# Performance work log

Hardware: AMD Instinct MI355X
Metric: run time of the kernel (lower is better)

## Reference

```python
import jax, jax.numpy as jnp
import numpy as np

N_NODES = 50000
N_EDGES = 800000
IN_CH = 64
HID = 128  # hidden_dim_conv == hidden_dim_readout


def setup_inputs() -> dict:
    key = jax.random.key(0)
    ks = jax.random.split(key, 16)
    x = jax.random.normal(ks[0], (N_NODES, 1, IN_CH), dtype=jnp.float32)
    edge_index = jax.random.randint(ks[1], (2, N_EDGES), 0, N_NODES, dtype=jnp.int64)
    edge_weight = jax.random.uniform(ks[2], (N_EDGES,), dtype=jnp.float32)

    def lin(k, out_d, in_d):
        s = 1.0 / np.sqrt(in_d)
        return jax.random.uniform(k, (out_d, in_d), minval=-s, maxval=s, dtype=jnp.float32)

    params = {
        "W_rel0": lin(ks[3], HID, IN_CH), "b_rel0": jnp.zeros((HID,), jnp.float32),
        "W_root0": lin(ks[4], HID, IN_CH),
        "W_ro0": lin(ks[5], HID, HID), "b_ro0": jnp.zeros((HID,), jnp.float32),
        "W_rel1": lin(ks[6], HID, HID), "b_rel1": jnp.zeros((HID,), jnp.float32),
        "W_root1": lin(ks[7], HID, HID),
        "W_ro1": lin(ks[8], HID, HID), "b_ro1": jnp.zeros((HID,), jnp.float32),
        "W_prd": lin(ks[9], 1, HID), "b_prd": jnp.zeros((1,), jnp.float32),
    }
    return {"dynamic_node_features": x, "edge_index": edge_index, "edge_weight": edge_weight, **params}


def reference(dynamic_node_features, edge_index, edge_weight,
              W_rel0, b_rel0, W_root0, W_ro0, b_ro0,
              W_rel1, b_rel1, W_root1, W_ro1, b_ro1,
              W_prd, b_prd):
    # Dropout layers are identity at inference.
    src, dst = edge_index[0], edge_index[1]
    n = dynamic_node_features.shape[0]
    # in-degree counts for 'mean' aggregation (nodes with no in-edges -> 0 output)
    counts = jax.ops.segment_sum(jnp.ones((edge_weight.shape[0],), edge_weight.dtype), dst, num_segments=n)
    denom = jnp.maximum(counts, 1.0)[:, None]  # [N,1]

    def graph_conv(h, W_rel, b_rel, W_root):
        # PyG GraphConv: lin_rel(mean_j edge_weight_ij * h_j) + lin_root(h_i)
        msg = edge_weight[:, None] * h[src]                       # [E,C]
        agg = jax.ops.segment_sum(msg, dst, num_segments=n) / denom  # [N,C]
        return agg @ W_rel.T + b_rel + h @ W_root.T

    h = dynamic_node_features[:, 0, :]                            # [N,IN_CH]
    h = jax.nn.relu(graph_conv(h, W_rel0, b_rel0, W_root0))
    h = jax.nn.relu(h @ W_ro0.T + b_ro0)                          # readout layer 0
    h = jax.nn.relu(graph_conv(h, W_rel1, b_rel1, W_root1))
    h = jax.nn.relu(h @ W_ro1.T + b_ro1)                          # readout layer 1
    out = h @ W_prd.T + b_prd                                     # [N,1]
    return out[:, None, :]                                        # [N,1,1]
```

## Files before the change

kernel.cpp:

```cpp
#include <hip/hip_runtime.h>
#include <hip/hip_fp16.h>

#define N_NODES 50000
#define N_EDGES 800000
#define IN_CH 64
#define HID 128
#define MAXDEG 64
#define CHUNK 6250

typedef __attribute__((ext_vector_type(8))) short bf16x8;
typedef __attribute__((ext_vector_type(8))) _Float16 f16x8;
typedef __attribute__((ext_vector_type(4))) float f32x4;

__device__ __forceinline__ unsigned pack_split(float v) {
    unsigned u = __float_as_uint(v);
    unsigned hi = (u + 0x7fffu + ((u >> 16) & 1u)) & 0xffff0000u;
    float r = v - __uint_as_float(hi);
    unsigned ur = __float_as_uint(r);
    unsigned lo = ((ur + 0x7fffu + ((ur >> 16) & 1u)) >> 16) & 0xffffu;
    return hi | lo;
}


__global__ __launch_bounds__(256) void count_fill_pack(
    const int* __restrict__ src, const int* __restrict__ dst,
    const float* __restrict__ w, int* __restrict__ cnt, int2* __restrict__ csr, int e,
    const float* __restrict__ x, __half* __restrict__ xh, int nx,
    const float* __restrict__ w_rel0, const float* __restrict__ w_root0,
    const float* __restrict__ w_ro0, const float* __restrict__ w_rel1,
    const float* __restrict__ w_root1, const float* __restrict__ w_ro1,
    unsigned short* __restrict__ hi, unsigned short* __restrict__ lo,
    unsigned short* __restrict__ rhi, unsigned short* __restrict__ rlo) {
    const int cls = (int)blockIdx.x & 7;
    const int slice = (int)blockIdx.x >> 3;
    const int nsl = (int)gridDim.x >> 3;
    const int tid = (int)(blockIdx.x * blockDim.x + threadIdx.x);

    for (int i = slice * 256 + (int)threadIdx.x; i < e; i += nsl * 256) {
        int d = dst[i];
        if (d / CHUNK != cls) continue;
        int r = atomicAdd(&cnt[d], 1);
        if (r < MAXDEG) {
            unsigned long long v =
                ((unsigned long long)(unsigned)__float_as_uint(w[i]) << 32) | (unsigned)src[i];
            __builtin_nontemporal_store(v, (unsigned long long*)&csr[(size_t)d * MAXDEG + r]);
        }
    }

    int i4 = tid * 4;
    if (i4 + 3 < nx) {
        float4 v = *(const float4*)&x[i4];
        __half2 a = __floats2half2_rn(v.x, v.y);
        __half2 b = __floats2half2_rn(v.z, v.w);
        uint2 o;
        o.x = *(unsigned*)&a;
        o.y = *(unsigned*)&b;
        *(uint2*)&xh[i4] = o;
    }

    if (tid < 81920) {
        const float* srcw;
        int li;
        if (tid < 8192) { srcw = w_rel0; li = tid; }
        else if (tid < 16384) { srcw = w_root0; li = tid - 8192; }
        else if (tid < 32768) { srcw = w_ro0; li = tid - 16384; }
        else if (tid < 49152) { srcw = w_rel1; li = tid - 32768; }
        else if (tid < 65536) { srcw = w_root1; li = tid - 49152; }
        else { srcw = w_ro1; li = tid - 65536; }
        unsigned p = pack_split(srcw[li]);
        hi[tid] = (unsigned short)(p >> 16);
        lo[tid] = (unsigned short)(p & 0xffffu);
    } else if (tid < 90112) {
        int li = tid - 81920;
        float v = w_root0[li];
        __half h = __float2half(v);
        __half l = __float2half(v - __half2float(h));
        rhi[li] = __half_as_ushort(h);
        rlo[li] = __half_as_ushort(l);
    } else if (tid < 106496) {
        int li = tid - 90112;
        float v = w_root1[li];
        __half h = __float2half(v);
        __half l = __float2half(v - __half2float(h));
        rhi[8192 + li] = __half_as_ushort(h);
        rlo[8192 + li] = __half_as_ushort(l);
    }
}


__global__ void aggregate64(const __half2* __restrict__ xh2, const int* __restrict__ cnt,
                            const int2* __restrict__ csr,
                            unsigned* __restrict__ agg, int n) {
    int tid = blockIdx.x * blockDim.x + threadIdx.x;
    int lane = tid & 63;
    int sl = lane & 31;
    int node = ((tid >> 6) << 1) + (lane >> 5);
    if (node >= n) return;
    int deg = cnt[node];
    int end = deg < MAXDEG ? deg : MAXDEG;
    float inv = 1.0f / fmaxf((float)deg, 1.0f);
    const int2* cp = csr + (size_t)node * MAXDEG;
    float ax = 0.0f, ay = 0.0f;
    int e = 0;
    for (; e + 16 <= end; e += 16) {
        int2 p[16];
        __half2 v[16];
#pragma unroll
        for (int q = 0; q < 16; ++q) p[q] = cp[e + q];
#pragma unroll
        for (int q = 0; q < 16; ++q) v[q] = xh2[(size_t)p[q].x * 32 + sl];
#pragma unroll
        for (int q = 0; q < 16; ++q) {
            float wv = __int_as_float(p[q].y);
            float2 f = __half22float2(v[q]);
            ax += wv * f.x;
            ay += wv * f.y;
        }
    }
    for (; e + 4 <= end; e += 4) {
        int2 p[4];
        __half2 v[4];
#pragma unroll
        for (int q = 0; q < 4; ++q) p[q] = cp[e + q];
#pragma unroll
        for (int q = 0; q < 4; ++q) v[q] = xh2[(size_t)p[q].x * 32 + sl];
#pragma unroll
        for (int q = 0; q < 4; ++q) {
            float wv = __int_as_float(p[q].y);
            float2 f = __half22float2(v[q]);
            ax += wv * f.x;
            ay += wv * f.y;
        }
    }
    for (; e < end; ++e) {
        int2 p = cp[e];
        float wv = __int_as_float(p.y);
        float2 f = __half22float2(xh2[(size_t)p.x * 32 + sl]);
        ax += wv * f.x;
        ay += wv * f.y;
    }
    uint2 o;
    o.x = pack_split(ax * inv);
    o.y = pack_split(ay * inv);
    ((uint2*)agg)[(size_t)node * 32 + sl] = o;
}

__global__ void aggregate128(const uint2* __restrict__ h2h, const int* __restrict__ cnt,
                             const int2* __restrict__ csr,
                             unsigned* __restrict__ agg, int n) {
    int tid = blockIdx.x * blockDim.x + threadIdx.x;
    int lane = tid & 63;
    int sl = lane & 31;
    int node = ((tid >> 6) << 1) + (lane >> 5);
    if (node >= n) return;
    int deg = cnt[node];
    int end = deg < MAXDEG ? deg : MAXDEG;
    float inv = 1.0f / fmaxf((float)deg, 1.0f);
    const int2* cp = csr + (size_t)node * MAXDEG;
    float ax = 0.0f, ay = 0.0f, az = 0.0f, aw = 0.0f;
    int e = 0;
    for (; e + 8 <= end; e += 8) {
        int2 p[8];
        uint2 v[8];
#pragma unroll
        for (int q = 0; q < 8; ++q) p[q] = cp[e + q];
#pragma unroll
        for (int q = 0; q < 8; ++q) v[q] = h2h[(size_t)p[q].x * 32 + sl];
#pragma unroll
        for (int q = 0; q < 8; ++q) {
            float wv = __int_as_float(p[q].y);
            float2 f0 = __half22float2(*(const __half2*)&v[q].x);
            float2 f1 = __half22float2(*(const __half2*)&v[q].y);
            ax += wv * f0.x;
            ay += wv * f0.y;
            az += wv * f1.x;
            aw += wv * f1.y;
        }
    }
    for (; e < end; ++e) {
        int2 p = cp[e];
        float wv = __int_as_float(p.y);
        uint2 v = h2h[(size_t)p.x * 32 + sl];
        float2 f0 = __half22float2(*(const __half2*)&v.x);
        float2 f1 = __half22float2(*(const __half2*)&v.y);
        ax += wv * f0.x;
        ay += wv * f0.y;
        az += wv * f1.x;
        aw += wv * f1.y;
    }
    uint4 o;
    o.x = pack_split(ax * inv);
    o.y = pack_split(ay * inv);
    o.z = pack_split(az * inv);
    o.w = pack_split(aw * inv);
    *(uint4*)&agg[(size_t)node * 128 + sl * 4] = o;
}


template <int K1, int EMIT2>
__global__ __launch_bounds__(256) void gemm_fused(
    const unsigned* __restrict__ A0,
    const unsigned short* __restrict__ W0Hi, const unsigned short* __restrict__ W0Lo,
    const __half* __restrict__ A1h,
    const unsigned short* __restrict__ W1fHi, const unsigned short* __restrict__ W1fLo,
    const float* __restrict__ bias1,
    const unsigned short* __restrict__ W2Hi, const unsigned short* __restrict__ W2Lo,
    const float* __restrict__ bias2,
    __half* __restrict__ Yh,
    const float* __restrict__ pred_w, const float* __restrict__ pred_b,
    float* __restrict__ pred_out, int n) {
    constexpr int KS1 = K1 / 32;
    constexpr int KS2 = 128 / 32;
    const int lane = (int)threadIdx.x & 63;
    const int wv = (int)threadIdx.x >> 6;
    const int col = lane & 15;
    const int quad = lane >> 4;

    __shared__ unsigned h1s[16][132];
    __shared__ float pp[4][16];

    bf16x8 wh1[2][KS1], wl1[2][KS1];
    f16x8 wf1h[2][KS1], wf1l[2][KS1];
    bf16x8 wh2[2][KS2], wl2[2][KS2];
#pragma unroll
    for (int tt = 0; tt < 2; ++tt) {
        const int j = (2 * wv + tt) * 16 + col;
#pragma unroll
        for (int ks = 0; ks < KS1; ++ks) {
            const size_t wo = (size_t)j * K1 + ks * 32 + quad * 8;
            wh1[tt][ks] = *(const bf16x8*)&W0Hi[wo];
            wl1[tt][ks] = *(const bf16x8*)&W0Lo[wo];
            wf1h[tt][ks] = *(const f16x8*)&W1fHi[wo];
            wf1l[tt][ks] = *(const f16x8*)&W1fLo[wo];
        }
#pragma unroll
        for (int ks = 0; ks < KS2; ++ks) {
            const size_t wo = (size_t)j * 128 + ks * 32 + quad * 8;
            wh2[tt][ks] = *(const bf16x8*)&W2Hi[wo];
            wl2[tt][ks] = *(const bf16x8*)&W2Lo[wo];
        }
    }

    float bb1[2], bb2[2], wpv[2];
#pragma unroll
    for (int tt = 0; tt < 2; ++tt) {
        bb1[tt] = bias1[(2 * wv + tt) * 16 + col];
        bb2[tt] = bias2[(2 * wv + tt) * 16 + col];
        if constexpr (EMIT2 == 2) wpv[tt] = pred_w[(2 * wv + tt) * 16 + col];
    }

    const int ngroups = (n + 15) >> 4;
    for (int g = (int)blockIdx.x; g < ngroups; g += (int)gridDim.x) {
        const int m0 = g * 16;
        int arow = m0 + col;
        if (arow >= n) arow = n - 1;

        f32x4 acc[2];
#pragma unroll
        for (int tt = 0; tt < 2; ++tt) acc[tt] = (f32x4){0.f, 0.f, 0.f, 0.f};
#pragma unroll
        for (int ks = 0; ks < KS1; ++ks) {
            const unsigned* ap = &A0[(size_t)arow * K1 + ks * 32 + quad * 8];
            uint4 q0 = *(const uint4*)ap;
            uint4 q1 = *(const uint4*)(ap + 4);
            bf16x8 ahi, alo;
            ahi[0] = (short)(q0.x >> 16); alo[0] = (short)(q0.x & 0xffffu);
            ahi[1] = (short)(q0.y >> 16); alo[1] = (short)(q0.y & 0xffffu);
            ahi[2] = (short)(q0.z >> 16); alo[2] = (short)(q0.z & 0xffffu);
            ahi[3] = (short)(q0.w >> 16); alo[3] = (short)(q0.w & 0xffffu);
            ahi[4] = (short)(q1.x >> 16); alo[4] = (short)(q1.x & 0xffffu);
            ahi[5] = (short)(q1.y >> 16); alo[5] = (short)(q1.y & 0xffffu);
            ahi[6] = (short)(q1.z >> 16); alo[6] = (short)(q1.z & 0xffffu);
            ahi[7] = (short)(q1.w >> 16); alo[7] = (short)(q1.w & 0xffffu);
#pragma unroll
            for (int tt = 0; tt < 2; ++tt) {
                acc[tt] = __builtin_amdgcn_mfma_f32_16x16x32_bf16(ahi, wh1[tt][ks], acc[tt], 0, 0, 0);
                acc[tt] = __builtin_amdgcn_mfma_f32_16x16x32_bf16(ahi, wl1[tt][ks], acc[tt], 0, 0, 0);
                acc[tt] = __builtin_amdgcn_mfma_f32_16x16x32_bf16(alo, wh1[tt][ks], acc[tt], 0, 0, 0);
            }
        }
#pragma unroll
        for (int ks = 0; ks < KS1; ++ks) {
            f16x8 af = *(const f16x8*)&A1h[(size_t)arow * K1 + ks * 32 + quad * 8];
#pragma unroll
            for (int tt = 0; tt < 2; ++tt) {
                acc[tt] = __builtin_amdgcn_mfma_f32_16x16x32_f16(af, wf1h[tt][ks], acc[tt], 0, 0, 0);
                acc[tt] = __builtin_amdgcn_mfma_f32_16x16x32_f16(af, wf1l[tt][ks], acc[tt], 0, 0, 0);
            }
        }
#pragma unroll
        for (int tt = 0; tt < 2; ++tt)
#pragma unroll
            for (int r = 0; r < 4; ++r) {
                float y = fmaxf(acc[tt][r] + bb1[tt], 0.f);
                h1s[quad * 4 + r][(2 * wv + tt) * 16 + col] = pack_split(y);
            }
        __syncthreads();

        f32x4 acc2[2];
#pragma unroll
        for (int tt = 0; tt < 2; ++tt) acc2[tt] = (f32x4){0.f, 0.f, 0.f, 0.f};
#pragma unroll
        for (int ks = 0; ks < KS2; ++ks) {
            const uint4* lp = (const uint4*)&h1s[col][ks * 32 + quad * 8];
            uint4 q0 = lp[0];
            uint4 q1 = lp[1];
            bf16x8 ahi, alo;
            ahi[0] = (short)(q0.x >> 16); alo[0] = (short)(q0.x & 0xffffu);
            ahi[1] = (short)(q0.y >> 16); alo[1] = (short)(q0.y & 0xffffu);
            ahi[2] = (short)(q0.z >> 16); alo[2] = (short)(q0.z & 0xffffu);
            ahi[3] = (short)(q0.w >> 16); alo[3] = (short)(q0.w & 0xffffu);
            ahi[4] = (short)(q1.x >> 16); alo[4] = (short)(q1.x & 0xffffu);
            ahi[5] = (short)(q1.y >> 16); alo[5] = (short)(q1.y & 0xffffu);
            ahi[6] = (short)(q1.z >> 16); alo[6] = (short)(q1.z & 0xffffu);
            ahi[7] = (short)(q1.w >> 16); alo[7] = (short)(q1.w & 0xffffu);
#pragma unroll
            for (int tt = 0; tt < 2; ++tt) {
                acc2[tt] = __builtin_amdgcn_mfma_f32_16x16x32_bf16(ahi, wh2[tt][ks], acc2[tt], 0, 0, 0);
                acc2[tt] = __builtin_amdgcn_mfma_f32_16x16x32_bf16(ahi, wl2[tt][ks], acc2[tt], 0, 0, 0);
                acc2[tt] = __builtin_amdgcn_mfma_f32_16x16x32_bf16(alo, wh2[tt][ks], acc2[tt], 0, 0, 0);
            }
        }

        float yv[2][4];
#pragma unroll
        for (int tt = 0; tt < 2; ++tt)
#pragma unroll
            for (int r = 0; r < 4; ++r)
                yv[tt][r] = fmaxf(acc2[tt][r] + bb2[tt], 0.f);

        if constexpr (EMIT2 == 1) {
#pragma unroll
            for (int tt = 0; tt < 2; ++tt) {
                const int j = (2 * wv + tt) * 16 + col;
#pragma unroll
                for (int r = 0; r < 4; ++r) {
                    int node = m0 + quad * 4 + r;
                    if (node >= n) continue;
                    Yh[(size_t)node * 128 + j] = __float2half(yv[tt][r]);
                }
            }
        } else {
            float pr[4];
#pragma unroll
            for (int r = 0; r < 4; ++r) pr[r] = yv[0][r] * wpv[0] + yv[1][r] * wpv[1];
#pragma unroll
            for (int off = 8; off > 0; off >>= 1)
#pragma unroll
                for (int r = 0; r < 4; ++r) pr[r] += __shfl_down(pr[r], off);
            if (col == 0) {
#pragma unroll
                for (int r = 0; r < 4; ++r) pp[wv][quad * 4 + r] = pr[r];
            }
            __syncthreads();
            if (wv == 0 && lane < 16) {
                int node = m0 + lane;
                if (node < n)
                    pred_out[node] = pp[0][lane] + pp[1][lane] + pp[2][lane] + pp[3][lane] + pred_b[0];
            }
        }
        __syncthreads();
    }
}


extern "C" void kernel_launch(void* const* d_in, const int* in_sizes, int n_in,
                              void* d_out, int out_size, void* d_ws, size_t ws_size,
                              hipStream_t stream) {
    const float* x = (const float*)d_in[0];
    const int* edge_index = (const int*)d_in[1];
    const float* edge_w = (const float*)d_in[2];
    const float* W_rel0 = (const float*)d_in[3];
    const float* b_rel0 = (const float*)d_in[4];
    const float* W_root0 = (const float*)d_in[5];
    const float* W_ro0 = (const float*)d_in[6];
    const float* b_ro0 = (const float*)d_in[7];
    const float* W_rel1 = (const float*)d_in[8];
    const float* b_rel1 = (const float*)d_in[9];
    const float* W_root1 = (const float*)d_in[10];
    const float* W_ro1 = (const float*)d_in[11];
    const float* b_ro1 = (const float*)d_in[12];
    const float* W_prd = (const float*)d_in[13];
    const float* b_prd = (const float*)d_in[14];
    float* out = (float*)d_out;

    const int* e_src = edge_index;
    const int* e_dst = edge_index + N_EDGES;

    char* ws = (char*)d_ws;
    size_t off = 0;
    auto alloc = [&](size_t bytes) {
        char* p = ws + off;
        off += (bytes + 255) & ~(size_t)255;
        return p;
    };
    int* cnt = (int*)alloc(N_NODES * 4);
    int2* csr = (int2*)alloc((size_t)N_NODES * MAXDEG * 8);
    unsigned short* WHI = (unsigned short*)alloc(81920 * 2);
    unsigned short* WLO = (unsigned short*)alloc(81920 * 2);
    unsigned short* RHI = (unsigned short*)alloc(24576 * 2);
    unsigned short* RLO = (unsigned short*)alloc(24576 * 2);
    __half* xh = (__half*)alloc((size_t)N_NODES * 64 * 2);
    unsigned* AGGp = (unsigned*)alloc((size_t)N_NODES * 128 * 4);
    __half* H2h = (__half*)alloc((size_t)N_NODES * 128 * 2);

    hipMemsetAsync(cnt, 0, N_NODES * 4, stream);

    const int NX = N_NODES * 64;
    count_fill_pack<<<3200, 256, 0, stream>>>(
        e_src, e_dst, edge_w, cnt, csr, N_EDGES,
        x, xh, NX, W_rel0, W_root0, W_ro0, W_rel1, W_root1, W_ro1, WHI, WLO, RHI, RLO);

    const int AGGB2 = (((N_NODES + 1) / 2) * 64 + 255) / 256;
    const int GGRID = 512;

    aggregate64<<<AGGB2, 256, 0, stream>>>((const __half2*)xh, cnt, csr, AGGp, N_NODES);
    gemm_fused<64, 1><<<GGRID, 256, 0, stream>>>(
        AGGp, WHI + 0, WLO + 0, xh, RHI + 0, RLO + 0, b_rel0,
        WHI + 16384, WLO + 16384, b_ro0,
        H2h, nullptr, nullptr, nullptr, N_NODES);
    aggregate128<<<AGGB2, 256, 0, stream>>>((const uint2*)H2h, cnt, csr, AGGp, N_NODES);
    gemm_fused<128, 2><<<GGRID, 256, 0, stream>>>(
        AGGp, WHI + 32768, WLO + 32768, H2h, RHI + 8192, RLO + 8192, b_rel1,
        WHI + 65536, WLO + 65536, b_ro1,
        nullptr, W_prd, b_prd, out, N_NODES);
}
```

Measured before the change: 252.8 us.

## Fuse neighbor aggregation into per-layer GEMM kernel via shared memory

The separate aggregate kernels are removed. Each 16-node group now gathers its neighbors' half-precision features inside the fused GEMM kernel, writes the split hi/lo aggregates to shared memory, and feeds the MFMA stage from there. This avoids writing and re-reading the N x K1 x 4-byte aggregate buffer and saves two launches. In exchange the latency-bound gather runs inside a register-heavy kernel with a block barrier, which may reduce overlap, so the grid is raised to 1024 blocks.

```diff
diff --git a/kernel.cpp b/kernel.cpp
--- a/kernel.cpp
+++ b/kernel.cpp
@@ -88,118 +88,10 @@
 }
 
 
-__global__ void aggregate64(const __half2* __restrict__ xh2, const int* __restrict__ cnt,
-                            const int2* __restrict__ csr,
-                            unsigned* __restrict__ agg, int n) {
-    int tid = blockIdx.x * blockDim.x + threadIdx.x;
-    int lane = tid & 63;
-    int sl = lane & 31;
-    int node = ((tid >> 6) << 1) + (lane >> 5);
-    if (node >= n) return;
-    int deg = cnt[node];
-    int end = deg < MAXDEG ? deg : MAXDEG;
-    float inv = 1.0f / fmaxf((float)deg, 1.0f);
-    const int2* cp = csr + (size_t)node * MAXDEG;
-    float ax = 0.0f, ay = 0.0f;
-    int e = 0;
-    for (; e + 16 <= end; e += 16) {
-        int2 p[16];
-        __half2 v[16];
-#pragma unroll
-        for (int q = 0; q < 16; ++q) p[q] = cp[e + q];
-#pragma unroll
-        for (int q = 0; q < 16; ++q) v[q] = xh2[(size_t)p[q].x * 32 + sl];
-#pragma unroll
-        for (int q = 0; q < 16; ++q) {
-            float wv = __int_as_float(p[q].y);
-            float2 f = __half22float2(v[q]);
-            ax += wv * f.x;
-            ay += wv * f.y;
-        }
-    }
-    for (; e + 4 <= end; e += 4) {
-        int2 p[4];
-        __half2 v[4];
-#pragma unroll
-        for (int q = 0; q < 4; ++q) p[q] = cp[e + q];
-#pragma unroll
-        for (int q = 0; q < 4; ++q) v[q] = xh2[(size_t)p[q].x * 32 + sl];
-#pragma unroll
-        for (int q = 0; q < 4; ++q) {
-            float wv = __int_as_float(p[q].y);
-            float2 f = __half22float2(v[q]);
-            ax += wv * f.x;
-            ay += wv * f.y;
-        }
-    }
-    for (; e < end; ++e) {
-        int2 p = cp[e];
-        float wv = __int_as_float(p.y);
-        float2 f = __half22float2(xh2[(size_t)p.x * 32 + sl]);
-        ax += wv * f.x;
-        ay += wv * f.y;
-    }
-    uint2 o;
-    o.x = pack_split(ax * inv);
-    o.y = pack_split(ay * inv);
-    ((uint2*)agg)[(size_t)node * 32 + sl] = o;
-}
-
-__global__ void aggregate128(const uint2* __restrict__ h2h, const int* __restrict__ cnt,
-                             const int2* __restrict__ csr,
-                             unsigned* __restrict__ agg, int n) {
-    int tid = blockIdx.x * blockDim.x + threadIdx.x;
-    int lane = tid & 63;
-    int sl = lane & 31;
-    int node = ((tid >> 6) << 1) + (lane >> 5);
-    if (node >= n) return;
-    int deg = cnt[node];
-    int end = deg < MAXDEG ? deg : MAXDEG;
-    float inv = 1.0f / fmaxf((float)deg, 1.0f);
-    const int2* cp = csr + (size_t)node * MAXDEG;
-    float ax = 0.0f, ay = 0.0f, az = 0.0f, aw = 0.0f;
-    int e = 0;
-    for (; e + 8 <= end; e += 8) {
-        int2 p[8];
-        uint2 v[8];
-#pragma unroll
-        for (int q = 0; q < 8; ++q) p[q] = cp[e + q];
-#pragma unroll
-        for (int q = 0; q < 8; ++q) v[q] = h2h[(size_t)p[q].x * 32 + sl];
-#pragma unroll
-        for (int q = 0; q < 8; ++q) {
-            float wv = __int_as_float(p[q].y);
-            float2 f0 = __half22float2(*(const __half2*)&v[q].x);
-            float2 f1 = __half22float2(*(const __half2*)&v[q].y);
-            ax += wv * f0.x;
-            ay += wv * f0.y;
-            az += wv * f1.x;
-            aw += wv * f1.y;
-        }
-    }
-    for (; e < end; ++e) {
-        int2 p = cp[e];
-        float wv = __int_as_float(p.y);
-        uint2 v = h2h[(size_t)p.x * 32 + sl];
-        float2 f0 = __half22float2(*(const __half2*)&v.x);
-        float2 f1 = __half22float2(*(const __half2*)&v.y);
-        ax += wv * f0.x;
-        ay += wv * f0.y;
-        az += wv * f1.x;
-        aw += wv * f1.y;
-    }
-    uint4 o;
-    o.x = pack_split(ax * inv);
-    o.y = pack_split(ay * inv);
-    o.z = pack_split(az * inv);
-    o.w = pack_split(aw * inv);
-    *(uint4*)&agg[(size_t)node * 128 + sl * 4] = o;
-}
-
-
 template <int K1, int EMIT2>
-__global__ __launch_bounds__(256) void gemm_fused(
-    const unsigned* __restrict__ A0,
+__global__ __launch_bounds__(256) void layer_fused(
+    const unsigned* __restrict__ gsrc,
+    const int* __restrict__ cnt, const int2* __restrict__ csr,
     const unsigned short* __restrict__ W0Hi, const unsigned short* __restrict__ W0Lo,
     const __half* __restrict__ A1h,
     const unsigned short* __restrict__ W1fHi, const unsigned short* __restrict__ W1fLo,
@@ -211,12 +103,14 @@
     float* __restrict__ pred_out, int n) {
     constexpr int KS1 = K1 / 32;
     constexpr int KS2 = 128 / 32;
+    constexpr int RU2 = K1 / 4;
     const int lane = (int)threadIdx.x & 63;
     const int wv = (int)threadIdx.x >> 6;
     const int col = lane & 15;
     const int quad = lane >> 4;
 
-    __shared__ unsigned h1s[16][132];
+    __shared__ __align__(16) unsigned aggs[16][K1 + 4];
+    __shared__ __align__(16) unsigned h1s[16][132];
     __shared__ float pp[4][16];
 
     bf16x8 wh1[2][KS1], wl1[2][KS1];
@@ -249,20 +143,74 @@
         if constexpr (EMIT2 == 2) wpv[tt] = pred_w[(2 * wv + tt) * 16 + col];
     }
 
+    const uint2* g2 = (const uint2*)gsrc;
     const int ngroups = (n + 15) >> 4;
     for (int g = (int)blockIdx.x; g < ngroups; g += (int)gridDim.x) {
         const int m0 = g * 16;
+
+        constexpr int NCON = 64 / RU2;
+        constexpr int NPASS = 4 / NCON;
+        const int slu = lane & (RU2 - 1);
+        const int nsub = lane / RU2;
+#pragma unroll
+        for (int pass = 0; pass < NPASS; ++pass) {
+            int nloc = wv * 4 + pass * NCON + nsub;
+            int node = m0 + nloc;
+            if (node >= n) node = n - 1;
+            int deg = cnt[node];
+            int end = deg < MAXDEG ? deg : MAXDEG;
+            float inv = 1.0f / fmaxf((float)deg, 1.0f);
+            const int2* cp = csr + (size_t)node * MAXDEG;
+            float ax = 0.f, ay = 0.f, az = 0.f, aw = 0.f;
+            int e = 0;
+            for (; e + 4 <= end; e += 4) {
+                int2 p[4];
+                uint2 v[4];
+#pragma unroll
+                for (int q = 0; q < 4; ++q) p[q] = cp[e + q];
+#pragma unroll
+                for (int q = 0; q < 4; ++q) v[q] = g2[(size_t)p[q].x * RU2 + slu];
+#pragma unroll
+                for (int q = 0; q < 4; ++q) {
+                    float wgt = __int_as_float(p[q].y);
+                    float2 f0 = __half22float2(*(const __half2*)&v[q].x);
+                    float2 f1 = __half22float2(*(const __half2*)&v[q].y);
+                    ax += wgt * f0.x;
+                    ay += wgt * f0.y;
+                    az += wgt * f1.x;
+                    aw += wgt * f1.y;
+                }
+            }
+            for (; e < end; ++e) {
+                int2 p = cp[e];
+                float wgt = __int_as_float(p.y);
+                uint2 v = g2[(size_t)p.x * RU2 + slu];
+                float2 f0 = __half22float2(*(const __half2*)&v.x);
+                float2 f1 = __half22float2(*(const __half2*)&v.y);
+                ax += wgt * f0.x;
+                ay += wgt * f0.y;
+                az += wgt * f1.x;
+                aw += wgt * f1.y;
+            }
+            uint4 o;
+            o.x = pack_split(ax * inv);
+            o.y = pack_split(ay * inv);
+            o.z = pack_split(az * inv);
+            o.w = pack_split(aw * inv);
+            *(uint4*)&aggs[nloc][slu * 4] = o;
+        }
+        __syncthreads();
+
         int arow = m0 + col;
         if (arow >= n) arow = n - 1;
-
         f32x4 acc[2];
 #pragma unroll
         for (int tt = 0; tt < 2; ++tt) acc[tt] = (f32x4){0.f, 0.f, 0.f, 0.f};
 #pragma unroll
         for (int ks = 0; ks < KS1; ++ks) {
-            const unsigned* ap = &A0[(size_t)arow * K1 + ks * 32 + quad * 8];
-            uint4 q0 = *(const uint4*)ap;
-            uint4 q1 = *(const uint4*)(ap + 4);
+            const uint4* lp = (const uint4*)&aggs[col][ks * 32 + quad * 8];
+            uint4 q0 = lp[0];
+            uint4 q1 = lp[1];
             bf16x8 ahi, alo;
             ahi[0] = (short)(q0.x >> 16); alo[0] = (short)(q0.x & 0xffffu);
             ahi[1] = (short)(q0.y >> 16); alo[1] = (short)(q0.y & 0xffffu);
@@ -401,7 +349,6 @@
     unsigned short* RHI = (unsigned short*)alloc(24576 * 2);
     unsigned short* RLO = (unsigned short*)alloc(24576 * 2);
     __half* xh = (__half*)alloc((size_t)N_NODES * 64 * 2);
-    unsigned* AGGp = (unsigned*)alloc((size_t)N_NODES * 128 * 4);
     __half* H2h = (__half*)alloc((size_t)N_NODES * 128 * 2);
 
     hipMemsetAsync(cnt, 0, N_NODES * 4, stream);
@@ -411,17 +358,16 @@
         e_src, e_dst, edge_w, cnt, csr, N_EDGES,
         x, xh, NX, W_rel0, W_root0, W_ro0, W_rel1, W_root1, W_ro1, WHI, WLO, RHI, RLO);
 
-    const int AGGB2 = (((N_NODES + 1) / 2) * 64 + 255) / 256;
-    const int GGRID = 512;
-
-    aggregate64<<<AGGB2, 256, 0, stream>>>((const __half2*)xh, cnt, csr, AGGp, N_NODES);
-    gemm_fused<64, 1><<<GGRID, 256, 0, stream>>>(
-        AGGp, WHI + 0, WLO + 0, xh, RHI + 0, RLO + 0, b_rel0,
+    const int GGRID = 1024;
+
+    layer_fused<64, 1><<<GGRID, 256, 0, stream>>>(
+        (const unsigned*)xh, cnt, csr,
+        WHI + 0, WLO + 0, xh, RHI + 0, RLO + 0, b_rel0,
         WHI + 16384, WLO + 16384, b_ro0,
         H2h, nullptr, nullptr, nullptr, N_NODES);
-    aggregate128<<<AGGB2, 256, 0, stream>>>((const uint2*)H2h, cnt, csr, AGGp, N_NODES);
-    gemm_fused<128, 2><<<GGRID, 256, 0, stream>>>(
-        AGGp, WHI + 32768, WLO + 32768, H2h, RHI + 8192, RLO + 8192, b_rel1,
+    layer_fused<128, 2><<<GGRID, 256, 0, stream>>>(
+        (const unsigned*)H2h, cnt, csr,
+        WHI + 32768, WLO + 32768, H2h, RHI + 8192, RLO + 8192, b_rel1,
         WHI + 65536, WLO + 65536, b_ro1,
         nullptr, W_prd, b_prd, out, N_NODES);
 }
```

New measurement: 350.7 us. 38.7% more time.
